# Kernel tuning notes

Measured on AMD Instinct MI355X. Metric: run time of the kernel, lower is better.

The kernel has to match this reference:

```python
import jax, jax.numpy as jnp
from jax import lax
import numpy as np

IMG = 640
C = 20  # num_classes
A = 3   # anchors per scale
LB, LO, LC = 0.05, 1.0, 0.5
ANCHORS = jnp.asarray(np.array([[(10, 13), (16, 30), (33, 23)],
                                [(30, 61), (62, 45), (59, 119)],
                                [(116, 90), (156, 198), (373, 326)]], dtype=np.float32) / IMG)


def bce_logits_mean(x, z):
    # BCEWithLogitsLoss (pos_weight=1): mean over all elements, numerically stable
    return jnp.mean(jnp.maximum(x, 0.0) - x * z + jnp.log1p(jnp.exp(-jnp.abs(x))))


def iou_cxcywh(b1, b2, eps=1e-7):
    # b1, b2: [..., 4] in (cx, cy, w, h)
    b1x1 = b1[..., 0] - b1[..., 2] / 2; b1y1 = b1[..., 1] - b1[..., 3] / 2
    b1x2 = b1[..., 0] + b1[..., 2] / 2; b1y2 = b1[..., 1] + b1[..., 3] / 2
    b2x1 = b2[..., 0] - b2[..., 2] / 2; b2y1 = b2[..., 1] - b2[..., 3] / 2
    b2x2 = b2[..., 0] + b2[..., 2] / 2; b2y2 = b2[..., 1] + b2[..., 3] / 2
    iw = jnp.clip(jnp.minimum(b1x2, b2x2) - jnp.maximum(b1x1, b2x1), 0.0)
    ih = jnp.clip(jnp.minimum(b1y2, b2y2) - jnp.maximum(b1y1, b2y1), 0.0)
    inter = iw * ih
    union = (b1x2 - b1x1) * (b1y2 - b1y1) + (b2x2 - b2x1) * (b2y2 - b2y1) - inter + eps
    return inter / union


def build_target(targets, anchors, stride, H, W):
    # targets: [N, T, 6] = (x1, y1, x2, y2, obj, cls); anchors: [A, 2]
    N, T, _ = targets.shape
    x1, y1, x2, y2 = targets[..., 0], targets[..., 1], targets[..., 2], targets[..., 3]
    cls = targets[..., 5]
    valid = (x2 > x1) & (y2 > y1)
    cx = (x1 + x2) * 0.5; cy = (y1 + y2) * 0.5
    bw = x2 - x1; bh = y2 - y1
    gx = jnp.clip(cx / stride, 0.0, W - 1).astype(jnp.int32)  # trunc == floor (nonneg)
    gy = jnp.clip(cy / stride, 0.0, H - 1).astype(jnp.int32)
    dx = cx / stride - gx; dy = cy / stride - gy
    # anchor match: min(r, 1/r) product, argmax over A
    r = jnp.stack([bw[..., None] / anchors[:, 0], bh[..., None] / anchors[:, 1]], axis=-1)  # [N,T,A,2]
    iou_like = jnp.prod(jnp.minimum(r, 1.0 / (r + 1e-6)), axis=-1)  # [N,T,A]
    best = jnp.argmax(iou_like, axis=-1)  # [N,T]
    aw = anchors[best, 0]; ah = anchors[best, 1]
    cls_i = cls.astype(jnp.int32)
    cls_ok = ((cls_i >= 0) & (cls_i < C)).astype(jnp.float32)
    onehot = jax.nn.one_hot(jnp.clip(cls_i, 0, C - 1), C) * cls_ok[..., None]  # [N,T,C]
    vals = jnp.concatenate([
        jnp.stack([dx + 0.5, dy + 0.5, bw / aw, bh / ah, jnp.ones_like(dx)], axis=-1),
        onehot], axis=-1)  # [N,T,5+C]
    tt = jnp.zeros((N, A, 5 + C, H, W), jnp.float32)
    bidx = jnp.arange(N)

    def step(tensor, xs):
        v, gxt, gyt, bt, vt = xs  # per-target slice across the batch, [N,...]
        old = tensor[bidx, bt, :, gyt, gxt]  # [N, 5+C]
        new = jnp.where(vt[:, None], v, old)
        return tensor.at[bidx, bt, :, gyt, gxt].set(new), None

    xs = (jnp.swapaxes(vals, 0, 1), gx.T, gy.T, best.T, valid.T)
    tt, _ = lax.scan(step, tt, xs)
    return tt


def loss_per_scale(pred, targets, scale_idx):
    stride = (8, 16, 32)[scale_idx]
    H = W = IMG // stride
    anchors = ANCHORS[scale_idx]
    N = pred.shape[0]
    tt = build_target(targets, anchors, float(stride), H, W)  # [N,A,5+C,H,W]
    pred = pred.reshape(N, A, 5 + C, H, W)
    ygrid, xgrid = jnp.meshgrid(jnp.arange(H, dtype=jnp.float32),
                                jnp.arange(W, dtype=jnp.float32), indexing='ij')
    grid = jnp.stack([xgrid, ygrid], axis=-1)[None, None]  # [1,1,H,W,2]
    p_txty = jnp.moveaxis(pred[:, :, 0:2], 2, -1)  # [N,A,H,W,2]
    p_twth = jnp.moveaxis(pred[:, :, 2:4], 2, -1)
    p_xy = (2.0 * jax.nn.sigmoid(p_txty) - 0.5 + grid) * stride
    p_wh = (2.0 * jax.nn.sigmoid(p_twth)) ** 2 * anchors.reshape(1, A, 1, 1, 2) * stride
    t_txty = jnp.moveaxis(tt[:, :, 0:2], 2, -1)
    t_twth = jnp.moveaxis(tt[:, :, 2:4], 2, -1)
    t_xy = (t_txty + grid) * stride
    t_wh = t_twth ** 2 * anchors.reshape(1, A, 1, 1, 2)  # NOTE: no *stride, as in source
    pred_box = jnp.concatenate([p_xy, p_wh], axis=-1)
    tgt_box = jnp.concatenate([t_xy, t_wh], axis=-1)
    pos = tt[:, :, 4] == 1.0  # [N,A,H,W]
    npos = jnp.sum(pos)
    ious = iou_cxcywh(pred_box, tgt_box)
    loss_box = jnp.sum((1.0 - ious) * pos) / jnp.maximum(npos, 1).astype(jnp.float32)
    loss_obj = bce_logits_mean(pred[:, :, 4], tt[:, :, 4])
    loss_cls = jnp.where(npos > 0, bce_logits_mean(pred[:, :, 5:], tt[:, :, 5:]), 0.0)
    total = LB * loss_box + LO * loss_obj + LC * loss_cls
    return total, loss_box, loss_obj, loss_cls


def setup_inputs() -> dict:
    key = jax.random.key(0)
    k = jax.random.split(key, 7)
    N, T = 32, 60
    p0 = jax.random.normal(k[0], (N, 75, 80, 80), jnp.float32)
    p1 = jax.random.normal(k[1], (N, 75, 40, 40), jnp.float32)
    p2 = jax.random.normal(k[2], (N, 75, 20, 20), jnp.float32)
    cxy = jax.random.uniform(k[3], (N, T, 2)) * IMG
    wh = jax.random.uniform(k[4], (N, T, 2)) * 120.0 + 8.0
    cls = jax.random.randint(k[5], (N, T), 0, C).astype(jnp.float32)
    x1 = jnp.clip(cxy[..., 0] - wh[..., 0] / 2, 0.0, IMG)
    x2 = jnp.clip(cxy[..., 0] + wh[..., 0] / 2, 0.0, IMG)
    y1 = jnp.clip(cxy[..., 1] - wh[..., 1] / 2, 0.0, IMG)
    y2 = jnp.clip(cxy[..., 1] + wh[..., 1] / 2, 0.0, IMG)
    targets = jnp.stack([x1, y1, x2, y2, jnp.ones_like(x1), cls], axis=-1)
    return {"p0": p0, "p1": p1, "p2": p2, "targets": targets}


def reference(p0, p1, p2, targets):
    total = jnp.float32(0.0)
    lb = jnp.float32(0.0); lo = jnp.float32(0.0); lc = jnp.float32(0.0)
    for i, p in enumerate((p0, p1, p2)):  # 3 structurally distinct scales
        t, b, o, c = loss_per_scale(p, targets, i)
        total = total + t; lb = lb + b; lo = lo + o; lc = lc + c
    return total, lb, lo, lc
```

## Files before the change

kernel.cpp:

```cpp
#include <hip/hip_runtime.h>


#define NB 32
#define NT 60
#define NC 20
#define THREADS 256

#define TGTB 96
#define DB0 1440
#define DB1 384
#define DB2 96
#define DENSB (DB0 + DB1 + DB2)
#define PB0 2240
#define PB12 2100

#define WS_DENSE 384

__constant__ float c_anch[3][3][2] = {
  {{10.f/640.f, 13.f/640.f}, {16.f/640.f, 30.f/640.f}, {33.f/640.f, 23.f/640.f}},
  {{30.f/640.f, 61.f/640.f}, {62.f/640.f, 45.f/640.f}, {59.f/640.f, 119.f/640.f}},
  {{116.f/640.f, 90.f/640.f}, {156.f/640.f, 198.f/640.f}, {373.f/640.f, 326.f/640.f}},
};

__device__ __forceinline__ float softplus0(float x) {
  return fmaxf(x, 0.f) + __logf(1.f + __expf(-fabsf(x)));
}
__device__ __forceinline__ float sp4(float4 v) {
  return softplus0(v.x) + softplus0(v.y) + softplus0(v.z) + softplus0(v.w);
}
__device__ __forceinline__ float sigm(float x) {
  return 1.f / (1.f + __expf(-x));
}

template<int HW, int BPG, int PB>
__device__ void sum_groups(const float* __restrict__ p, int d,
                           float* __restrict__ outp) {
  const int HW4 = HW / 4;
  int g = d / BPG;
  int sub = d - g * BPG;
  int n = g / 3;
  int a = g - n * 3;
  const float* bp = p + (size_t)(n * 75 + a * 25 + 4) * HW;
  int tid = threadIdx.x;
  int k0 = sub * PB + tid;
  float4 v[8];
#pragma unroll
  for (int u = 0; u < 8; ++u)
    v[u] = *reinterpret_cast<const float4*>(bp + 4 * (k0 + u * 256));
  const int TAIL = PB - 2048;
  bool hasTail = tid < TAIL;
  int kt = sub * PB + 2048 + tid;
  float4 vt = make_float4(0.f, 0.f, 0.f, 0.f);
  if (hasTail) vt = *reinterpret_cast<const float4*>(bp + 4 * kt);
  float accO = 0.f, accC = 0.f;
#pragma unroll
  for (int u = 0; u < 8; ++u) {
    float s = sp4(v[u]);
    bool isO = (k0 + u * 256) < HW4;
    accO += isO ? s : 0.f;
    accC += isO ? 0.f : s;
  }
  if (hasTail) {
    float s = sp4(vt);
    bool isO = kt < HW4;
    accO += isO ? s : 0.f;
    accC += isO ? 0.f : s;
  }
#pragma unroll
  for (int o = 32; o > 0; o >>= 1) {
    accO += __shfl_down(accO, o, 64);
    accC += __shfl_down(accC, o, 64);
  }
  __shared__ float sO[4], sC[4];
  int wid = threadIdx.x >> 6, lane = threadIdx.x & 63;
  if (lane == 0) { sO[wid] = accO; sC[wid] = accC; }
  __syncthreads();
  if (threadIdx.x == 0) {
    outp[0] = sO[0] + sO[1] + sO[2] + sO[3];
    outp[1] = sC[0] + sC[1] + sC[2] + sC[3];
  }
}

__device__ void target_block(const float* __restrict__ pred,
                             const float* __restrict__ tg,
                             int scale, int n, float* __restrict__ outp) {
  const int strd = 8 << scale;
  const int W = 80 >> scale;
  const int HW = W * W;
  __shared__ int s_key[64];
  __shared__ int s_val[64];
  int t = threadIdx.x;
  float boxterm = 0.f, objc = 0.f, clsc = 0.f, npos = 0.f;
  float bw = 0.f, bh = 0.f, dx = 0.f, dy = 0.f, clsf = 0.f;
  int gx = 0, gy = 0, best = 0;
  bool valid = false;
  if (t < 64) {
    if (t < NT) {
      const float* g = tg + ((size_t)n * NT + t) * 6;
      float x1 = g[0], y1 = g[1], x2 = g[2], y2 = g[3];
      clsf = g[5];
      valid = (x2 > x1) && (y2 > y1);
      float cx = (x1 + x2) * 0.5f, cy = (y1 + y2) * 0.5f;
      bw = x2 - x1; bh = y2 - y1;
      float fs = (float)strd;
      float gxf = cx / fs, gyf = cy / fs;
      float wm1 = (float)(W - 1);
      gx = (int)fminf(fmaxf(gxf, 0.f), wm1);
      gy = (int)fminf(fmaxf(gyf, 0.f), wm1);
      dx = gxf - (float)gx;
      dy = gyf - (float)gy;
      float bi = -1e30f;
      for (int a = 0; a < 3; a++) {
        float aw = c_anch[scale][a][0], ah = c_anch[scale][a][1];
        float rw = bw / aw, rh = bh / ah;
        float il = fminf(rw, 1.f / (rw + 1e-6f)) * fminf(rh, 1.f / (rh + 1e-6f));
        if (il > bi) { bi = il; best = a; }
      }
      s_key[t] = (best * W + gy) * W + gx;
      s_val[t] = valid ? 1 : 0;
    } else {
      s_key[t] = -1; s_val[t] = 0;
    }
  }
  __syncthreads();
  if (t < NT && valid) {
    bool win = true;
    int key = s_key[t];
    for (int u = t + 1; u < NT; ++u)
      if (s_val[u] && s_key[u] == key) { win = false; break; }
    if (win) {
      float aw = c_anch[scale][best][0], ah = c_anch[scale][best][1];
      const float* base = pred + (size_t)(n * 75 + best * 25) * HW + gy * W + gx;
      float tx = base[0];
      float ty = base[HW];
      float tw = base[2 * HW];
      float th = base[3 * HW];
      float ob = base[4 * HW];
      int clsi = (int)clsf;
      bool clsok = (clsi >= 0) && (clsi < NC);
      int clscl = clsi < 0 ? 0 : (clsi > NC - 1 ? NC - 1 : clsi);
      float cv = base[(5 + clscl) * HW];
      float fs = (float)strd;
      float px = (2.f * sigm(tx) - 0.5f + (float)gx) * fs;
      float py = (2.f * sigm(ty) - 0.5f + (float)gy) * fs;
      float sw = 2.f * sigm(tw); float pw = sw * sw * aw * fs;
      float sh = 2.f * sigm(th); float ph = sh * sh * ah * fs;
      float qx = ((dx + 0.5f) + (float)gx) * fs;
      float qy = ((dy + 0.5f) + (float)gy) * fs;
      float rw = bw / aw; float qw = rw * rw * aw;
      float rh = bh / ah; float qh = rh * rh * ah;
      float b1x1 = px - pw * 0.5f, b1x2 = px + pw * 0.5f;
      float b1y1 = py - ph * 0.5f, b1y2 = py + ph * 0.5f;
      float b2x1 = qx - qw * 0.5f, b2x2 = qx + qw * 0.5f;
      float b2y1 = qy - qh * 0.5f, b2y2 = qy + qh * 0.5f;
      float iw = fmaxf(fminf(b1x2, b2x2) - fmaxf(b1x1, b2x1), 0.f);
      float ih = fmaxf(fminf(b1y2, b2y2) - fmaxf(b1y1, b2y1), 0.f);
      float inter = iw * ih;
      float uni = (b1x2 - b1x1) * (b1y2 - b1y1)
                + (b2x2 - b2x1) * (b2y2 - b2y1) - inter + 1e-7f;
      float iou = inter / uni;
      boxterm = 1.f - iou;
      objc = -ob;
      clsc = clsok ? -cv : 0.f;
      npos = 1.f;
    }
  }
  if (t < 64) {
#pragma unroll
    for (int o = 32; o > 0; o >>= 1) {
      boxterm += __shfl_down(boxterm, o, 64);
      objc    += __shfl_down(objc, o, 64);
      clsc    += __shfl_down(clsc, o, 64);
      npos    += __shfl_down(npos, o, 64);
    }
    if (t == 0) {
      outp[0] = boxterm; outp[1] = objc; outp[2] = clsc; outp[3] = npos;
    }
  }
}

__global__ __launch_bounds__(THREADS)
void yolo_main(const float* __restrict__ p0, const float* __restrict__ p1,
               const float* __restrict__ p2, const float* __restrict__ tg,
               float* __restrict__ ws) {
  int b = blockIdx.x;
  if (b < TGTB) {
    int scale = b / NB, n = b - scale * NB;
    const float* p = scale == 0 ? p0 : (scale == 1 ? p1 : p2);
    target_block(p, tg, scale, n, ws + 4 * (size_t)b);
    return;
  }
  int d = b - TGTB;
  float* outp = ws + WS_DENSE + 2 * (size_t)d;
  if (d < DB0)            sum_groups<6400, 15, PB0>(p0, d, outp);
  else if (d < DB0 + DB1) sum_groups<1600, 4, PB12>(p1, d - DB0, outp);
  else                    sum_groups<400, 1, PB12>(p2, d - (DB0 + DB1), outp);
}

__global__ __launch_bounds__(THREADS)
void yolo_final(const float* __restrict__ ws, float* __restrict__ out) {
  int t = threadIdx.x;
  float2 dv[8];
#pragma unroll
  for (int r = 0; r < 7; ++r)
    dv[r] = *reinterpret_cast<const float2*>(ws + WS_DENSE + 2 * (size_t)(t + 256 * r));
  bool has7 = t < DENSB - 1792;
  dv[7] = make_float2(0.f, 0.f);
  if (has7)
    dv[7] = *reinterpret_cast<const float2*>(ws + WS_DENSE + 2 * (size_t)(t + 1792));
  float4 tv = make_float4(0.f, 0.f, 0.f, 0.f);
  if (t < TGTB)
    tv = *reinterpret_cast<const float4*>(ws + 4 * (size_t)t);

  float acc[18];
#pragma unroll
  for (int k = 0; k < 18; k++) acc[k] = 0.f;
#pragma unroll
  for (int r = 0; r < 8; ++r) {
    int b = t + 256 * r;
    int s = (b < DB0) ? 0 : (b < DB0 + DB1 ? 1 : 2);
    acc[2 * s] += dv[r].x;
    acc[2 * s + 1] += dv[r].y;
  }
  if (t < TGTB) {
    int s = t / NB;
    acc[6 + 4 * s + 0] += tv.x;
    acc[6 + 4 * s + 1] += tv.y;
    acc[6 + 4 * s + 2] += tv.z;
    acc[6 + 4 * s + 3] += tv.w;
  }
#pragma unroll
  for (int o = 32; o > 0; o >>= 1)
#pragma unroll
    for (int k = 0; k < 18; k++) acc[k] += __shfl_down(acc[k], o, 64);
  __shared__ float red[4][18];
  int wid = t >> 6, lane = t & 63;
  if (lane == 0)
#pragma unroll
    for (int k = 0; k < 18; k++) red[wid][k] = acc[k];
  __syncthreads();
  if (t == 0) {
    float r[18];
#pragma unroll
    for (int k = 0; k < 18; k++)
      r[k] = red[0][k] + red[1][k] + red[2][k] + red[3][k];
    const float objDen[3] = {614400.f, 153600.f, 38400.f};
    float total = 0.f, lb = 0.f, lo = 0.f, lc = 0.f;
    for (int s = 0; s < 3; s++) {
      float np = r[6 + 4 * s + 3];
      float lbs = r[6 + 4 * s + 0] / fmaxf(np, 1.f);
      float los = (r[2 * s] + r[6 + 4 * s + 1]) / objDen[s];
      float lcs = (np > 0.f)
                    ? (r[2 * s + 1] + r[6 + 4 * s + 2]) / (objDen[s] * (float)NC)
                    : 0.f;
      total += 0.05f * lbs + 1.0f * los + 0.5f * lcs;
      lb += lbs; lo += los; lc += lcs;
    }
    out[0] = total; out[1] = lb; out[2] = lo; out[3] = lc;
  }
}

extern "C" void kernel_launch(void* const* d_in, const int* in_sizes, int n_in,
                              void* d_out, int out_size, void* d_ws, size_t ws_size,
                              hipStream_t stream) {
  const float* p0 = (const float*)d_in[0];
  const float* p1 = (const float*)d_in[1];
  const float* p2 = (const float*)d_in[2];
  const float* tg = (const float*)d_in[3];
  float* ws = (float*)d_ws;
  yolo_main<<<TGTB + DENSB, THREADS, 0, stream>>>(p0, p1, p2, tg, ws);
  yolo_final<<<1, THREADS, 0, stream>>>(ws, (float*)d_out);
}
```

Before: 23.20 us.

## Fuse final reduction into main kernel via last-block atomic counter

Replaces the separate single-block finalize kernel with a last-block-done pattern. Each block publishes its partials with relaxed agent-scope atomic stores, waits on vmcnt, then bumps a global counter, and the block that sees the final count runs the finalize reduction. The intent is to remove the second kernel launch and its launch gap. In exchange it adds a hipMemsetAsync per call and relies on relaxed atomics plus a waitcnt for ordering, which is a subtle memory-model risk.

Measured after the change: 43.88 us. 89.2% more time.

```diff
diff --git a/kernel.cpp b/kernel.cpp
--- a/kernel.cpp
+++ b/kernel.cpp
@@ -11,10 +11,14 @@
 #define DB1 384
 #define DB2 96
 #define DENSB (DB0 + DB1 + DB2)
+#define TOTALB (TGTB + DENSB)
 #define PB0 2240
 #define PB12 2100
 
 #define WS_DENSE 384
+#define CNT_IDX 4224
+
+#define SCOPE_AGENT __HIP_MEMORY_SCOPE_AGENT
 
 __constant__ float c_anch[3][3][2] = {
   {{10.f/640.f, 13.f/640.f}, {16.f/640.f, 30.f/640.f}, {33.f/640.f, 23.f/640.f}},
@@ -30,6 +34,16 @@
 }
 __device__ __forceinline__ float sigm(float x) {
   return 1.f / (1.f + __expf(-x));
+}
+__device__ __forceinline__ void store2_rlx(float* p, float a, float b) {
+  union { float f[2]; unsigned long long u; } pk;
+  pk.f[0] = a; pk.f[1] = b;
+  __hip_atomic_store((unsigned long long*)p, pk.u, __ATOMIC_RELAXED, SCOPE_AGENT);
+}
+__device__ __forceinline__ float2 load2_rlx(const float* p) {
+  union { unsigned long long u; float f[2]; } pk;
+  pk.u = __hip_atomic_load((const unsigned long long*)p, __ATOMIC_RELAXED, SCOPE_AGENT);
+  return make_float2(pk.f[0], pk.f[1]);
 }
 
 template<int HW, int BPG, int PB>
@@ -75,10 +89,9 @@
   int wid = threadIdx.x >> 6, lane = threadIdx.x & 63;
   if (lane == 0) { sO[wid] = accO; sC[wid] = accC; }
   __syncthreads();
-  if (threadIdx.x == 0) {
-    outp[0] = sO[0] + sO[1] + sO[2] + sO[3];
-    outp[1] = sC[0] + sC[1] + sC[2] + sC[3];
-  }
+  if (threadIdx.x == 0)
+    store2_rlx(outp, sO[0] + sO[1] + sO[2] + sO[3],
+                     sC[0] + sC[1] + sC[2] + sC[3]);
 }
 
 __device__ void target_block(const float* __restrict__ pred,
@@ -174,44 +187,26 @@
       npos    += __shfl_down(npos, o, 64);
     }
     if (t == 0) {
-      outp[0] = boxterm; outp[1] = objc; outp[2] = clsc; outp[3] = npos;
-    }
-  }
-}
-
-__global__ __launch_bounds__(THREADS)
-void yolo_main(const float* __restrict__ p0, const float* __restrict__ p1,
-               const float* __restrict__ p2, const float* __restrict__ tg,
-               float* __restrict__ ws) {
-  int b = blockIdx.x;
-  if (b < TGTB) {
-    int scale = b / NB, n = b - scale * NB;
-    const float* p = scale == 0 ? p0 : (scale == 1 ? p1 : p2);
-    target_block(p, tg, scale, n, ws + 4 * (size_t)b);
-    return;
-  }
-  int d = b - TGTB;
-  float* outp = ws + WS_DENSE + 2 * (size_t)d;
-  if (d < DB0)            sum_groups<6400, 15, PB0>(p0, d, outp);
-  else if (d < DB0 + DB1) sum_groups<1600, 4, PB12>(p1, d - DB0, outp);
-  else                    sum_groups<400, 1, PB12>(p2, d - (DB0 + DB1), outp);
-}
-
-__global__ __launch_bounds__(THREADS)
-void yolo_final(const float* __restrict__ ws, float* __restrict__ out) {
+      store2_rlx(outp, boxterm, objc);
+      store2_rlx(outp + 2, clsc, npos);
+    }
+  }
+}
+
+__device__ void finalize(const float* __restrict__ ws, float* __restrict__ out) {
   int t = threadIdx.x;
   float2 dv[8];
 #pragma unroll
   for (int r = 0; r < 7; ++r)
-    dv[r] = *reinterpret_cast<const float2*>(ws + WS_DENSE + 2 * (size_t)(t + 256 * r));
+    dv[r] = load2_rlx(ws + WS_DENSE + 2 * (size_t)(t + 256 * r));
   bool has7 = t < DENSB - 1792;
   dv[7] = make_float2(0.f, 0.f);
-  if (has7)
-    dv[7] = *reinterpret_cast<const float2*>(ws + WS_DENSE + 2 * (size_t)(t + 1792));
-  float4 tv = make_float4(0.f, 0.f, 0.f, 0.f);
-  if (t < TGTB)
-    tv = *reinterpret_cast<const float4*>(ws + 4 * (size_t)t);
-
+  if (has7) dv[7] = load2_rlx(ws + WS_DENSE + 2 * (size_t)(t + 1792));
+  float2 ta = make_float2(0.f, 0.f), tb = make_float2(0.f, 0.f);
+  if (t < TGTB) {
+    ta = load2_rlx(ws + 4 * (size_t)t);
+    tb = load2_rlx(ws + 4 * (size_t)t + 2);
+  }
   float acc[18];
 #pragma unroll
   for (int k = 0; k < 18; k++) acc[k] = 0.f;
@@ -224,10 +219,10 @@
   }
   if (t < TGTB) {
     int s = t / NB;
-    acc[6 + 4 * s + 0] += tv.x;
-    acc[6 + 4 * s + 1] += tv.y;
-    acc[6 + 4 * s + 2] += tv.z;
-    acc[6 + 4 * s + 3] += tv.w;
+    acc[6 + 4 * s + 0] += ta.x;
+    acc[6 + 4 * s + 1] += ta.y;
+    acc[6 + 4 * s + 2] += tb.x;
+    acc[6 + 4 * s + 3] += tb.y;
   }
 #pragma unroll
   for (int o = 32; o > 0; o >>= 1)
@@ -260,6 +255,33 @@
   }
 }
 
+__global__ __launch_bounds__(THREADS)
+void yolo_main(const float* __restrict__ p0, const float* __restrict__ p1,
+               const float* __restrict__ p2, const float* __restrict__ tg,
+               float* __restrict__ ws, float* __restrict__ out,
+               unsigned int* __restrict__ cnt) {
+  int b = blockIdx.x;
+  if (b < TGTB) {
+    int scale = b / NB, n = b - scale * NB;
+    const float* p = scale == 0 ? p0 : (scale == 1 ? p1 : p2);
+    target_block(p, tg, scale, n, ws + 4 * (size_t)b);
+  } else {
+    int d = b - TGTB;
+    float* outp = ws + WS_DENSE + 2 * (size_t)d;
+    if (d < DB0)            sum_groups<6400, 15, PB0>(p0, d, outp);
+    else if (d < DB0 + DB1) sum_groups<1600, 4, PB12>(p1, d - DB0, outp);
+    else                    sum_groups<400, 1, PB12>(p2, d - (DB0 + DB1), outp);
+  }
+  __shared__ unsigned int s_last;
+  if (threadIdx.x == 0) {
+    asm volatile("s_waitcnt vmcnt(0)" ::: "memory");
+    unsigned int old = __hip_atomic_fetch_add(cnt, 1u, __ATOMIC_RELAXED, SCOPE_AGENT);
+    s_last = (old == (unsigned int)(TOTALB - 1)) ? 1u : 0u;
+  }
+  __syncthreads();
+  if (s_last) finalize(ws, out);
+}
+
 extern "C" void kernel_launch(void* const* d_in, const int* in_sizes, int n_in,
                               void* d_out, int out_size, void* d_ws, size_t ws_size,
                               hipStream_t stream) {
@@ -268,6 +290,8 @@
   const float* p2 = (const float*)d_in[2];
   const float* tg = (const float*)d_in[3];
   float* ws = (float*)d_ws;
-  yolo_main<<<TGTB + DENSB, THREADS, 0, stream>>>(p0, p1, p2, tg, ws);
-  yolo_final<<<1, THREADS, 0, stream>>>(ws, (float*)d_out);
-}
+  unsigned int* cnt = (unsigned int*)(ws + CNT_IDX);
+  hipMemsetAsync(cnt, 0, 4, stream);
+  yolo_main<<<TOTALB, THREADS, 0, stream>>>(p0, p1, p2, tg, ws,
+                                            (float*)d_out, cnt);
+}
```
